# Optimization experiments

Measured on AMD Instinct MI355X. Metric: run time of the kernel, lower is better.

Reference implementation:

```python
import jax, jax.numpy as jnp
import numpy as np

NUM_HEADS = 32
NUM_KV_HEADS = 8
HEAD_DIM = 128  # hidden_size 4096 / 32 heads
ROPE_BASE = 10000.0


def setup_inputs() -> dict:
    key = jax.random.key(0)
    ks = jax.random.split(key, 5)
    H = NUM_HEADS * HEAD_DIM
    KV = NUM_KV_HEADS * HEAD_DIM
    B, S = 1, 2048
    s = 0.02
    return {
        "hidden_states": jax.random.normal(ks[0], (B, S, H), dtype=jnp.float32),
        "Wq": jax.random.normal(ks[1], (H, H), dtype=jnp.float32) * s,
        "Wk": jax.random.normal(ks[2], (H, KV), dtype=jnp.float32) * s,
        "Wv": jax.random.normal(ks[3], (H, KV), dtype=jnp.float32) * s,
        "Wo": jax.random.normal(ks[4], (H, H), dtype=jnp.float32) * s,
    }


def _rope_tables(seq_len, head_dim, dtype):
    inv_freq = 1.0 / (ROPE_BASE ** (jnp.arange(0, head_dim, 2, dtype=jnp.float32) / head_dim))
    freqs = jnp.arange(seq_len, dtype=jnp.float32)[:, None] * inv_freq[None, :]  # [S, hd/2]
    emb = jnp.concatenate([freqs, freqs], axis=-1)  # [S, hd]
    return emb.astype(dtype)  # angles; cos/sin taken by caller


def _rotate_half(x):
    x1, x2 = jnp.split(x, 2, axis=-1)
    return jnp.concatenate([-x2, x1], axis=-1)


def reference(hidden_states, Wq, Wk, Wv, Wo):
    B, S, H = hidden_states.shape
    hd = HEAD_DIM
    scale = hd ** -0.5

    q = (hidden_states @ Wq).reshape(B, S, NUM_HEADS, hd).transpose(0, 2, 1, 3)      # [B,nh,S,hd]
    k = (hidden_states @ Wk).reshape(B, S, NUM_KV_HEADS, hd).transpose(0, 2, 1, 3)   # [B,nkv,S,hd]
    v = (hidden_states @ Wv).reshape(B, S, NUM_KV_HEADS, hd).transpose(0, 2, 1, 3)

    ang = _rope_tables(S, hd, hidden_states.dtype)          # [S, hd]
    cos = jnp.cos(ang)[None, None]                          # [1,1,S,hd]
    sin = jnp.sin(ang)[None, None]
    q = q * cos + _rotate_half(q) * sin
    k = k * cos + _rotate_half(k) * sin

    rep = NUM_HEADS // NUM_KV_HEADS
    if rep > 1:
        k = jnp.repeat(k, rep, axis=1)  # matches torch repeat_interleave on head dim
        v = jnp.repeat(v, rep, axis=1)

    scores = jnp.einsum("bhqd,bhkd->bhqk", q, k) * scale    # [B,nh,S,S]
    causal = jnp.triu(jnp.ones((S, S), dtype=bool), k=1)
    scores = jnp.where(causal[None, None], jnp.float32(-jnp.inf).astype(scores.dtype), scores)
    weights = jax.nn.softmax(scores, axis=-1)
    attn = jnp.einsum("bhqk,bhkd->bhqd", weights, v)        # [B,nh,S,hd]
    out = attn.transpose(0, 2, 1, 3).reshape(B, S, H) @ Wo  # [B,S,H]
    return (out, k, v)
```

## Files before the change

kernel.cpp:

```cpp
#include <hip/hip_runtime.h>
#include <hip/hip_bf16.h>
#include <math.h>

typedef __bf16 bf16_t;
typedef bf16_t bf16x8 __attribute__((ext_vector_type(8)));
typedef bf16_t bf16x4 __attribute__((ext_vector_type(4)));
typedef float  f32x4  __attribute__((ext_vector_type(4)));

#define AS1(p) ((__attribute__((address_space(1))) void*)(p))
#define AS3(p) ((__attribute__((address_space(3))) void*)(p))

__global__ void convert_f32_bf16(const float* __restrict__ in, bf16_t* __restrict__ out)
{
    int i = blockIdx.x * 256 + threadIdx.x;
    float4 v = ((const float4*)in)[i];
    bf16x4 o;
    o[0] = (bf16_t)v.x; o[1] = (bf16_t)v.y; o[2] = (bf16_t)v.z; o[3] = (bf16_t)v.w;
    ((bf16x4*)out)[i] = o;
}

__global__ void transpose_convert(const float* __restrict__ W, bf16_t* __restrict__ Wt,
                                  int K, int N)
{
    __shared__ float tile[32][33];
    const int n0 = blockIdx.x * 32;
    const int k0 = blockIdx.y * 32;
    const int r = threadIdx.x >> 5;
    const int c = threadIdx.x & 31;
    #pragma unroll
    for (int i = 0; i < 32; i += 8)
        tile[r + i][c] = W[(size_t)(k0 + r + i) * N + n0 + c];
    __syncthreads();
    #pragma unroll
    for (int i = 0; i < 32; i += 8)
        Wt[(size_t)(n0 + r + i) * K + k0 + c] = (bf16_t)tile[c][r + i];
}

template <typename OutT>
__global__ __launch_bounds__(512, 2)
void gemm_bt_256(const bf16_t* __restrict__ A, const bf16_t* __restrict__ Bt,
                 OutT* __restrict__ C, int M, int N, int K)
{
    __shared__ __align__(16) bf16_t As[2 * 256 * 64];
    __shared__ __align__(16) bf16_t Bs[2 * 256 * 64];

    const int tid  = threadIdx.x;
    const int wave = tid >> 6;
    const int lane = tid & 63;
    const int lm = lane & 15, lq = lane >> 4;
    const int wr = wave >> 2, wc = wave & 3;
    const int m0 = blockIdx.x * 256;
    const int n0 = blockIdx.y * 256;

    const int sr = tid >> 3;
    const int sg = ((tid & 7) ^ (sr & 7)) * 8;
    char* Ab = (char*)As;
    char* Bb = (char*)Bs;
    const int fl = lm * 128 + ((lq ^ (lm & 7)) << 4);

    const int NT = K >> 6;

#define STAGE_A(buf, kt, h) do {                                                              \
    const bf16_t* _g0 = A + (size_t)(m0 + (h) * 128 + sr) * K + (kt) * 64 + sg;               \
    const bf16_t* _g1 = A + (size_t)(m0 + (h) * 128 + 64 + sr) * K + (kt) * 64 + sg;          \
    __builtin_amdgcn_global_load_lds(AS1(_g0),                                                \
        AS3(Ab + (buf) * 32768 + ((h) * 128 + wave * 8) * 128), 16, 0, 0);                    \
    __builtin_amdgcn_global_load_lds(AS1(_g1),                                                \
        AS3(Ab + (buf) * 32768 + ((h) * 128 + 64 + wave * 8) * 128), 16, 0, 0);               \
} while (0)
#define STAGE_B(buf, kt, h) do {                                                              \
    const bf16_t* _g0 = Bt + (size_t)(n0 + (h) * 128 + sr) * K + (kt) * 64 + sg;              \
    const bf16_t* _g1 = Bt + (size_t)(n0 + (h) * 128 + 64 + sr) * K + (kt) * 64 + sg;         \
    __builtin_amdgcn_global_load_lds(AS1(_g0),                                                \
        AS3(Bb + (buf) * 32768 + ((h) * 128 + wave * 8) * 128), 16, 0, 0);                    \
    __builtin_amdgcn_global_load_lds(AS1(_g1),                                                \
        AS3(Bb + (buf) * 32768 + ((h) * 128 + 64 + wave * 8) * 128), 16, 0, 0);               \
} while (0)

    f32x4 acc[8][4] = {};

    STAGE_A(0, 0, 0); STAGE_A(0, 0, 1);
    STAGE_B(0, 0, 0); STAGE_B(0, 0, 1);
    if (NT > 1) STAGE_A(1, 1, 0);
    asm volatile("s_waitcnt vmcnt(2)" ::: "memory");
    __builtin_amdgcn_s_barrier();

    int cur = 0;
    for (int kt = 0; kt < NT; ++kt) {
        const int nxt = cur ^ 1;
        const char* Ac = Ab + cur * 32768;
        const char* Bc = Bb + cur * 32768;
        bf16x8 a0[4][2], a1[4][2], b0[2][2], b1[2][2];

        #pragma unroll
        for (int mf = 0; mf < 4; ++mf)
            #pragma unroll
            for (int kk = 0; kk < 2; ++kk)
                a0[mf][kk] = *(const bf16x8*)(Ac + (wr * 128 + mf * 16) * 128 + (fl ^ (kk << 6)));
        #pragma unroll
        for (int nf = 0; nf < 2; ++nf)
            #pragma unroll
            for (int kk = 0; kk < 2; ++kk)
                b0[nf][kk] = *(const bf16x8*)(Bc + (wc * 64 + nf * 16) * 128 + (fl ^ (kk << 6)));
        if (kt + 1 < NT) { STAGE_A(nxt, kt + 1, 1); STAGE_B(nxt, kt + 1, 0); }
        __builtin_amdgcn_s_barrier();
        asm volatile("s_waitcnt lgkmcnt(0)" ::: "memory");
        __builtin_amdgcn_s_setprio(1);
        #pragma unroll
        for (int mf = 0; mf < 4; ++mf)
            #pragma unroll
            for (int nf = 0; nf < 2; ++nf)
                #pragma unroll
                for (int kk = 0; kk < 2; ++kk)
                    acc[mf][nf] = __builtin_amdgcn_mfma_f32_16x16x32_bf16(
                        a0[mf][kk], b0[nf][kk], acc[mf][nf], 0, 0, 0);
        __builtin_amdgcn_s_setprio(0);
        __builtin_amdgcn_s_barrier();

        #pragma unroll
        for (int nf = 0; nf < 2; ++nf)
            #pragma unroll
            for (int kk = 0; kk < 2; ++kk)
                b1[nf][kk] = *(const bf16x8*)(Bc + (wc * 64 + 32 + nf * 16) * 128 + (fl ^ (kk << 6)));
        if (kt + 1 < NT) STAGE_B(nxt, kt + 1, 1);
        __builtin_amdgcn_s_barrier();
        asm volatile("s_waitcnt lgkmcnt(0)" ::: "memory");
        __builtin_amdgcn_s_setprio(1);
        #pragma unroll
        for (int mf = 0; mf < 4; ++mf)
            #pragma unroll
            for (int nf = 0; nf < 2; ++nf)
                #pragma unroll
                for (int kk = 0; kk < 2; ++kk)
                    acc[mf][2 + nf] = __builtin_amdgcn_mfma_f32_16x16x32_bf16(
                        a0[mf][kk], b1[nf][kk], acc[mf][2 + nf], 0, 0, 0);
        __builtin_amdgcn_s_setprio(0);
        __builtin_amdgcn_s_barrier();

        #pragma unroll
        for (int mf = 0; mf < 4; ++mf)
            #pragma unroll
            for (int kk = 0; kk < 2; ++kk)
                a1[mf][kk] = *(const bf16x8*)(Ac + (wr * 128 + 64 + mf * 16) * 128 + (fl ^ (kk << 6)));
        __builtin_amdgcn_s_barrier();
        asm volatile("s_waitcnt lgkmcnt(0)" ::: "memory");
        __builtin_amdgcn_s_setprio(1);
        #pragma unroll
        for (int mf = 0; mf < 4; ++mf)
            #pragma unroll
            for (int nf = 0; nf < 2; ++nf)
                #pragma unroll
                for (int kk = 0; kk < 2; ++kk)
                    acc[4 + mf][nf] = __builtin_amdgcn_mfma_f32_16x16x32_bf16(
                        a1[mf][kk], b0[nf][kk], acc[4 + mf][nf], 0, 0, 0);
        __builtin_amdgcn_s_setprio(0);
        __builtin_amdgcn_s_barrier();

        if (kt + 2 < NT) {
            STAGE_A(cur, kt + 2, 0);
            asm volatile("s_waitcnt vmcnt(2)" ::: "memory");
        } else {
            asm volatile("s_waitcnt vmcnt(0)" ::: "memory");
        }
        __builtin_amdgcn_s_barrier();
        __builtin_amdgcn_s_setprio(1);
        #pragma unroll
        for (int mf = 0; mf < 4; ++mf)
            #pragma unroll
            for (int nf = 0; nf < 2; ++nf)
                #pragma unroll
                for (int kk = 0; kk < 2; ++kk)
                    acc[4 + mf][2 + nf] = __builtin_amdgcn_mfma_f32_16x16x32_bf16(
                        a1[mf][kk], b1[nf][kk], acc[4 + mf][2 + nf], 0, 0, 0);
        __builtin_amdgcn_s_setprio(0);
        __builtin_amdgcn_s_barrier();
        cur = nxt;
    }
#undef STAGE_A
#undef STAGE_B

    #pragma unroll
    for (int mi = 0; mi < 8; ++mi) {
        #pragma unroll
        for (int ni = 0; ni < 4; ++ni) {
            const int row = m0 + wr * 128 + mi * 16 + lq * 4;
            const int col = n0 + wc * 64 + ni * 16 + lm;
            #pragma unroll
            for (int r = 0; r < 4; ++r) {
                float v = acc[mi][ni][r];
                if constexpr (sizeof(OutT) == 2)
                    C[(size_t)(row + r) * N + col] = (OutT)(bf16_t)v;
                else
                    C[(size_t)(row + r) * N + col] = v;
            }
        }
    }
}

__global__ void rope_qk(bf16_t* __restrict__ QKV, float* __restrict__ k_out, int S)
{
    int idx  = blockIdx.x * 256 + threadIdx.x;
    int d    = idx & 63;
    int s    = idx >> 6;
    int head = blockIdx.y;
    float ang = (float)s * exp2f((float)d * -0.20762050593f);
    float sn, cs;
    sincosf(ang, &sn, &cs);
    int col = head < 32 ? head * 128 : 4096 + (head - 32) * 128;
    bf16_t* p = QKV + (size_t)s * 6144 + col;
    float x1 = (float)p[d], x2 = (float)p[d + 64];
    float y1 = x1 * cs - x2 * sn;
    float y2 = x2 * cs + x1 * sn;
    p[d]      = (bf16_t)y1;
    p[d + 64] = (bf16_t)y2;
    if (head >= 32) {
        int g = head - 32;
        #pragma unroll
        for (int j = 0; j < 4; ++j) {
            float* kb = k_out + ((size_t)(g * 4 + j) * S + s) * 128;
            kb[d]      = y1;
            kb[d + 64] = y2;
        }
    }
}

__global__ void v_finish(const bf16_t* __restrict__ QKV, float* __restrict__ v_out,
                         bf16_t* __restrict__ Vt, int S)
{
    __shared__ bf16_t tl[32][33];
    const int s0  = blockIdx.x * 32;
    const int gd0 = blockIdx.y * 32;
    const int r = threadIdx.x >> 5;
    const int c = threadIdx.x & 31;
    #pragma unroll
    for (int i = 0; i < 32; i += 8) {
        int s = s0 + r + i;
        bf16_t v = QKV[(size_t)s * 6144 + 5120 + gd0 + c];
        tl[r + i][c] = v;
        int gd = gd0 + c;
        int g = gd >> 7, d = gd & 127;
        float vf = (float)v;
        #pragma unroll
        for (int j = 0; j < 4; ++j)
            v_out[((size_t)(g * 4 + j) * S + s) * 128 + d] = vf;
    }
    __syncthreads();
    #pragma unroll
    for (int i = 0; i < 32; i += 8)
        Vt[(size_t)(gd0 + r + i) * S + s0 + c] = tl[c][r + i];
}

__global__ void pack_frags(const bf16_t* __restrict__ QKV, const bf16_t* __restrict__ Vt,
                           bf16_t* __restrict__ Kfrag, bf16_t* __restrict__ Vfrag, int S)
{
    const int b  = blockIdx.x;
    const int g  = b >> 5, kt = b & 31;
    const int t  = threadIdx.x;
    bf16x8* Kf = (bf16x8*)Kfrag + (size_t)b * 1024;
    bf16x8* Vf = (bf16x8*)Vfrag + (size_t)b * 1024;
    #pragma unroll
    for (int i = 0; i < 4; ++i) {
        int slot = i * 256 + t;
        int f = slot >> 6, l = slot & 63;
        int kk = f >> 2, nt = f & 3, lm = l & 15, lq = l >> 4;
        Kf[slot] = *(const bf16x8*)(QKV + (size_t)(kt * 64 + nt * 16 + lm) * 6144
                                    + 4096 + g * 128 + kk * 32 + lq * 8);
    }
    #pragma unroll
    for (int i = 0; i < 4; ++i) {
        int slot = i * 256 + t;
        int f = slot >> 6, l = slot & 63;
        int kk = f >> 3, nt = f & 7, lm = l & 15, lq = l >> 4;
        Vf[slot] = *(const bf16x8*)(Vt + (size_t)(g * 128 + nt * 16 + lm) * S
                                    + kt * 64 + kk * 32 + lq * 8);
    }
}

__global__ __launch_bounds__(64, 2)
void attn_fwd(const bf16_t* __restrict__ QKV,
              const bf16_t* __restrict__ Kfrag, const bf16_t* __restrict__ Vfrag,
              bf16_t* __restrict__ O, int S)
{
    const int task = blockIdx.x;
    const int h    = task & 31;
    const int c    = 63 - (task >> 5);
    const int g    = h >> 2;
    const int lane = threadIdx.x;
    const int lm   = lane & 15;
    const int lq   = lane >> 4;
    const int q0   = c * 32;

    __shared__ bf16_t P[32 * 72];

    bf16x8 aq[2][4];
    #pragma unroll
    for (int mi = 0; mi < 2; ++mi) {
        const bf16_t* qrow = QKV + (size_t)(q0 + mi * 16 + lm) * 6144 + h * 128;
        #pragma unroll
        for (int kk = 0; kk < 4; ++kk)
            aq[mi][kk] = *(const bf16x8*)(qrow + kk * 32 + lq * 8);
    }

    f32x4 acc[2][8] = {};
    float mrow[2][4], lrow[2][4];
    #pragma unroll
    for (int mi = 0; mi < 2; ++mi)
        #pragma unroll
        for (int r = 0; r < 4; ++r) { mrow[mi][r] = -3.0e38f; lrow[mi][r] = 0.f; }
    const float scale = 0.08838834764831845f;

    const int nkt = (q0 >> 6) + 1;

    for (int kt = 0; kt < nkt; ++kt) {
        const int k0 = kt * 64;
        const bf16x8* Kf = (const bf16x8*)Kfrag + ((size_t)(g * 32 + kt) << 10);
        const bf16x8* Vf = (const bf16x8*)Vfrag + ((size_t)(g * 32 + kt) << 10);

        bf16x8 bk[4][4];
        #pragma unroll
        for (int kk = 0; kk < 4; ++kk)
            #pragma unroll
            for (int nt = 0; nt < 4; ++nt)
                bk[kk][nt] = Kf[(kk * 4 + nt) * 64 + lane];

        f32x4 sc[2][4] = {};
        #pragma unroll
        for (int kk = 0; kk < 4; ++kk)
            #pragma unroll
            for (int nt = 0; nt < 4; ++nt)
                #pragma unroll
                for (int mi = 0; mi < 2; ++mi)
                    sc[mi][nt] = __builtin_amdgcn_mfma_f32_16x16x32_bf16(
                        aq[mi][kk], bk[kk][nt], sc[mi][nt], 0, 0, 0);

        bf16x8 bv[2][8];
        #pragma unroll
        for (int kk = 0; kk < 2; ++kk)
            #pragma unroll
            for (int nt = 0; nt < 8; ++nt)
                bv[kk][nt] = Vf[(kk * 8 + nt) * 64 + lane];

        #pragma unroll
        for (int mi = 0; mi < 2; ++mi)
            #pragma unroll
            for (int nt = 0; nt < 4; ++nt)
                #pragma unroll
                for (int r = 0; r < 4; ++r)
                    sc[mi][nt][r] *= scale;

        if (kt == nkt - 1) {
            #pragma unroll
            for (int mi = 0; mi < 2; ++mi)
                #pragma unroll
                for (int nt = 0; nt < 4; ++nt) {
                    int col = k0 + nt * 16 + lm;
                    #pragma unroll
                    for (int r = 0; r < 4; ++r) {
                        int row = q0 + mi * 16 + lq * 4 + r;
                        if (col > row) sc[mi][nt][r] = -3.0e38f;
                    }
                }
        }

        #pragma unroll
        for (int mi = 0; mi < 2; ++mi) {
            float tmax[4];
            #pragma unroll
            for (int r = 0; r < 4; ++r)
                tmax[r] = fmaxf(fmaxf(sc[mi][0][r], sc[mi][1][r]),
                                fmaxf(sc[mi][2][r], sc[mi][3][r]));
            #pragma unroll
            for (int off = 1; off < 16; off <<= 1)
                #pragma unroll
                for (int r = 0; r < 4; ++r)
                    tmax[r] = fmaxf(tmax[r], __shfl_xor(tmax[r], off));

            float alpha[4];
            #pragma unroll
            for (int r = 0; r < 4; ++r) {
                float mn = fmaxf(mrow[mi][r], tmax[r]);
                alpha[r] = __expf(mrow[mi][r] - mn);
                mrow[mi][r] = mn;
            }
            float rsum[4] = {0.f, 0.f, 0.f, 0.f};
            #pragma unroll
            for (int nt = 0; nt < 4; ++nt)
                #pragma unroll
                for (int r = 0; r < 4; ++r) {
                    float p = __expf(sc[mi][nt][r] - mrow[mi][r]);
                    sc[mi][nt][r] = p;
                    rsum[r] += p;
                }
            #pragma unroll
            for (int off = 1; off < 16; off <<= 1)
                #pragma unroll
                for (int r = 0; r < 4; ++r)
                    rsum[r] += __shfl_xor(rsum[r], off);
            #pragma unroll
            for (int r = 0; r < 4; ++r)
                lrow[mi][r] = lrow[mi][r] * alpha[r] + rsum[r];
            #pragma unroll
            for (int nt = 0; nt < 8; ++nt)
                #pragma unroll
                for (int r = 0; r < 4; ++r)
                    acc[mi][nt][r] *= alpha[r];

            #pragma unroll
            for (int nt = 0; nt < 4; ++nt)
                #pragma unroll
                for (int r = 0; r < 4; ++r)
                    P[(mi * 16 + lq * 4 + r) * 72 + nt * 16 + lm] = (bf16_t)sc[mi][nt][r];
        }

        bf16x8 ap[2][2];
        #pragma unroll
        for (int mi = 0; mi < 2; ++mi)
            #pragma unroll
            for (int kk = 0; kk < 2; ++kk)
                ap[mi][kk] = *(const bf16x8*)(P + (mi * 16 + lm) * 72 + kk * 32 + lq * 8);

        #pragma unroll
        for (int kk = 0; kk < 2; ++kk)
            #pragma unroll
            for (int nt = 0; nt < 8; ++nt)
                #pragma unroll
                for (int mi = 0; mi < 2; ++mi)
                    acc[mi][nt] = __builtin_amdgcn_mfma_f32_16x16x32_bf16(
                        ap[mi][kk], bv[kk][nt], acc[mi][nt], 0, 0, 0);
    }

    #pragma unroll
    for (int mi = 0; mi < 2; ++mi) {
        float inv[4];
        #pragma unroll
        for (int r = 0; r < 4; ++r) inv[r] = 1.0f / lrow[mi][r];
        #pragma unroll
        for (int nt = 0; nt < 8; ++nt)
            #pragma unroll
            for (int r = 0; r < 4; ++r) {
                int row = q0 + mi * 16 + lq * 4 + r;
                O[(size_t)row * 4096 + h * 128 + nt * 16 + lm] =
                    (bf16_t)(acc[mi][nt][r] * inv[r]);
            }
    }
}

extern "C" void kernel_launch(void* const* d_in, const int* in_sizes, int n_in,
                              void* d_out, int out_size, void* d_ws, size_t ws_size,
                              hipStream_t stream)
{
    const float* hidden = (const float*)d_in[0];
    const float* Wq = (const float*)d_in[1];
    const float* Wk = (const float*)d_in[2];
    const float* Wv = (const float*)d_in[3];
    const float* Wo = (const float*)d_in[4];

    const int S = 2048, H = 4096, KV = 1024, NQKV = 6144;

    char* ws = (char*)d_ws;
    bf16_t* hid_b  = (bf16_t*)(ws);
    bf16_t* Wqkv_t = (bf16_t*)(ws + (size_t)(16u  << 20));
    bf16_t* Wo_t   = (bf16_t*)(ws + (size_t)(64u  << 20));
    bf16_t* QKV    = (bf16_t*)(ws + (size_t)(96u  << 20));
    bf16_t* Vt     = (bf16_t*)(ws + (size_t)(120u << 20));
    bf16_t* attn   = (bf16_t*)(ws + (size_t)(124u << 20));
    bf16_t* Kfrag  = (bf16_t*)(ws);
    bf16_t* Vfrag  = (bf16_t*)(ws + (size_t)(4u << 20));

    float* out_o = (float*)d_out;
    float* out_k = out_o + (size_t)S * H;
    float* out_v = out_k + (size_t)32 * S * 128;

    convert_f32_bf16<<<S * H / 4 / 256, 256, 0, stream>>>(hidden, hid_b);
    transpose_convert<<<dim3(H / 32, H / 32), 256, 0, stream>>>(Wq, Wqkv_t, H, H);
    transpose_convert<<<dim3(KV / 32, H / 32), 256, 0, stream>>>(Wk, Wqkv_t + (size_t)4096 * H, H, KV);
    transpose_convert<<<dim3(KV / 32, H / 32), 256, 0, stream>>>(Wv, Wqkv_t + (size_t)5120 * H, H, KV);
    transpose_convert<<<dim3(H / 32, H / 32), 256, 0, stream>>>(Wo, Wo_t, H, H);

    gemm_bt_256<bf16_t><<<dim3(S / 256, NQKV / 256), 512, 0, stream>>>(hid_b, Wqkv_t, QKV, S, NQKV, H);

    rope_qk<<<dim3(S * 64 / 256, 40), 256, 0, stream>>>(QKV, out_k, S);
    v_finish<<<dim3(S / 32, KV / 32), 256, 0, stream>>>(QKV, out_v, Vt, S);
    pack_frags<<<256, 256, 0, stream>>>(QKV, Vt, Kfrag, Vfrag, S);

    attn_fwd<<<2048, 64, 0, stream>>>(QKV, Kfrag, Vfrag, attn, S);

    gemm_bt_256<float><<<dim3(S / 256, H / 256), 512, 0, stream>>>(attn, Wo_t, out_o, S, H, H);
}
```

Measured before the change: 660.7 us.

## Split-K the output projection GEMM and restage the GEMM prefetch pipeline

```diff
diff --git a/kernel.cpp b/kernel.cpp
--- a/kernel.cpp
+++ b/kernel.cpp
@@ -19,6 +19,16 @@
     ((bf16x4*)out)[i] = o;
 }
 
+__global__ void add_f32(const float* __restrict__ a, const float* __restrict__ b,
+                        float* __restrict__ o)
+{
+    int i = blockIdx.x * 256 + threadIdx.x;
+    float4 x = ((const float4*)a)[i];
+    float4 y = ((const float4*)b)[i];
+    x.x += y.x; x.y += y.y; x.z += y.z; x.w += y.w;
+    ((float4*)o)[i] = x;
+}
+
 __global__ void transpose_convert(const float* __restrict__ W, bf16_t* __restrict__ Wt,
                                   int K, int N)
 {
@@ -39,7 +49,7 @@
 template <typename OutT>
 __global__ __launch_bounds__(512, 2)
 void gemm_bt_256(const bf16_t* __restrict__ A, const bf16_t* __restrict__ Bt,
-                 OutT* __restrict__ C, int M, int N, int K)
+                 OutT* __restrict__ C, int M, int N, int Kc, int Kld)
 {
     __shared__ __align__(16) bf16_t As[2 * 256 * 64];
     __shared__ __align__(16) bf16_t Bs[2 * 256 * 64];
@@ -51,6 +61,9 @@
     const int wr = wave >> 2, wc = wave & 3;
     const int m0 = blockIdx.x * 256;
     const int n0 = blockIdx.y * 256;
+    A  += (size_t)blockIdx.z * Kc;
+    Bt += (size_t)blockIdx.z * Kc;
+    C  += (size_t)blockIdx.z * M * N;
 
     const int sr = tid >> 3;
     const int sg = ((tid & 7) ^ (sr & 7)) * 8;
@@ -58,36 +71,40 @@
     char* Bb = (char*)Bs;
     const int fl = lm * 128 + ((lq ^ (lm & 7)) << 4);
 
-    const int NT = K >> 6;
+    const int NT = Kc >> 6;
 
 #define STAGE_A(buf, kt, h) do {                                                              \
-    const bf16_t* _g0 = A + (size_t)(m0 + (h) * 128 + sr) * K + (kt) * 64 + sg;               \
-    const bf16_t* _g1 = A + (size_t)(m0 + (h) * 128 + 64 + sr) * K + (kt) * 64 + sg;          \
+    const bf16_t* _g0 = A + (size_t)(m0 + (h) * 128 + sr) * Kld + (kt) * 64 + sg;             \
+    const bf16_t* _g1 = A + (size_t)(m0 + (h) * 128 + 64 + sr) * Kld + (kt) * 64 + sg;        \
     __builtin_amdgcn_global_load_lds(AS1(_g0),                                                \
         AS3(Ab + (buf) * 32768 + ((h) * 128 + wave * 8) * 128), 16, 0, 0);                    \
     __builtin_amdgcn_global_load_lds(AS1(_g1),                                                \
         AS3(Ab + (buf) * 32768 + ((h) * 128 + 64 + wave * 8) * 128), 16, 0, 0);               \
 } while (0)
 #define STAGE_B(buf, kt, h) do {                                                              \
-    const bf16_t* _g0 = Bt + (size_t)(n0 + (h) * 128 + sr) * K + (kt) * 64 + sg;              \
-    const bf16_t* _g1 = Bt + (size_t)(n0 + (h) * 128 + 64 + sr) * K + (kt) * 64 + sg;         \
+    const bf16_t* _g0 = Bt + (size_t)(n0 + (h) * 128 + sr) * Kld + (kt) * 64 + sg;            \
+    const bf16_t* _g1 = Bt + (size_t)(n0 + (h) * 128 + 64 + sr) * Kld + (kt) * 64 + sg;       \
     __builtin_amdgcn_global_load_lds(AS1(_g0),                                                \
         AS3(Bb + (buf) * 32768 + ((h) * 128 + wave * 8) * 128), 16, 0, 0);                    \
     __builtin_amdgcn_global_load_lds(AS1(_g1),                                                \
         AS3(Bb + (buf) * 32768 + ((h) * 128 + 64 + wave * 8) * 128), 16, 0, 0);               \
 } while (0)
+#define STAGE_TILE(buf, kt) do {                                                              \
+    STAGE_A(buf, kt, 0); STAGE_A(buf, kt, 1);                                                 \
+    STAGE_B(buf, kt, 0); STAGE_B(buf, kt, 1);                                                 \
+} while (0)
 
     f32x4 acc[8][4] = {};
 
-    STAGE_A(0, 0, 0); STAGE_A(0, 0, 1);
-    STAGE_B(0, 0, 0); STAGE_B(0, 0, 1);
-    if (NT > 1) STAGE_A(1, 1, 0);
-    asm volatile("s_waitcnt vmcnt(2)" ::: "memory");
-    __builtin_amdgcn_s_barrier();
+    STAGE_TILE(0, 0);
+    if (NT > 1) STAGE_TILE(1, 1);
 
     int cur = 0;
     for (int kt = 0; kt < NT; ++kt) {
-        const int nxt = cur ^ 1;
+        if (kt + 1 < NT) asm volatile("s_waitcnt vmcnt(8)" ::: "memory");
+        else             asm volatile("s_waitcnt vmcnt(0)" ::: "memory");
+        __builtin_amdgcn_s_barrier();
+
         const char* Ac = Ab + cur * 32768;
         const char* Bc = Bb + cur * 32768;
         bf16x8 a0[4][2], a1[4][2], b0[2][2], b1[2][2];
@@ -102,7 +119,6 @@
             #pragma unroll
             for (int kk = 0; kk < 2; ++kk)
                 b0[nf][kk] = *(const bf16x8*)(Bc + (wc * 64 + nf * 16) * 128 + (fl ^ (kk << 6)));
-        if (kt + 1 < NT) { STAGE_A(nxt, kt + 1, 1); STAGE_B(nxt, kt + 1, 0); }
         __builtin_amdgcn_s_barrier();
         asm volatile("s_waitcnt lgkmcnt(0)" ::: "memory");
         __builtin_amdgcn_s_setprio(1);
@@ -122,7 +138,6 @@
             #pragma unroll
             for (int kk = 0; kk < 2; ++kk)
                 b1[nf][kk] = *(const bf16x8*)(Bc + (wc * 64 + 32 + nf * 16) * 128 + (fl ^ (kk << 6)));
-        if (kt + 1 < NT) STAGE_B(nxt, kt + 1, 1);
         __builtin_amdgcn_s_barrier();
         asm volatile("s_waitcnt lgkmcnt(0)" ::: "memory");
         __builtin_amdgcn_s_setprio(1);
@@ -156,13 +171,7 @@
         __builtin_amdgcn_s_setprio(0);
         __builtin_amdgcn_s_barrier();
 
-        if (kt + 2 < NT) {
-            STAGE_A(cur, kt + 2, 0);
-            asm volatile("s_waitcnt vmcnt(2)" ::: "memory");
-        } else {
-            asm volatile("s_waitcnt vmcnt(0)" ::: "memory");
-        }
-        __builtin_amdgcn_s_barrier();
+        if (kt + 2 < NT) STAGE_TILE(cur, kt + 2);
         __builtin_amdgcn_s_setprio(1);
         #pragma unroll
         for (int mf = 0; mf < 4; ++mf)
@@ -173,11 +182,11 @@
                     acc[4 + mf][2 + nf] = __builtin_amdgcn_mfma_f32_16x16x32_bf16(
                         a1[mf][kk], b1[nf][kk], acc[4 + mf][2 + nf], 0, 0, 0);
         __builtin_amdgcn_s_setprio(0);
-        __builtin_amdgcn_s_barrier();
-        cur = nxt;
+        cur ^= 1;
     }
 #undef STAGE_A
 #undef STAGE_B
+#undef STAGE_TILE
 
     #pragma unroll
     for (int mi = 0; mi < 8; ++mi) {
@@ -466,6 +475,7 @@
     bf16_t* attn   = (bf16_t*)(ws + (size_t)(124u << 20));
     bf16_t* Kfrag  = (bf16_t*)(ws);
     bf16_t* Vfrag  = (bf16_t*)(ws + (size_t)(4u << 20));
+    float* slab0   = (float*)(ws);
 
     float* out_o = (float*)d_out;
     float* out_k = out_o + (size_t)S * H;
@@ -477,7 +487,8 @@
     transpose_convert<<<dim3(KV / 32, H / 32), 256, 0, stream>>>(Wv, Wqkv_t + (size_t)5120 * H, H, KV);
     transpose_convert<<<dim3(H / 32, H / 32), 256, 0, stream>>>(Wo, Wo_t, H, H);
 
-    gemm_bt_256<bf16_t><<<dim3(S / 256, NQKV / 256), 512, 0, stream>>>(hid_b, Wqkv_t, QKV, S, NQKV, H);
+    gemm_bt_256<bf16_t><<<dim3(S / 256, NQKV / 256, 1), 512, 0, stream>>>(
+        hid_b, Wqkv_t, QKV, S, NQKV, H, H);
 
     rope_qk<<<dim3(S * 64 / 256, 40), 256, 0, stream>>>(QKV, out_k, S);
     v_finish<<<dim3(S / 32, KV / 32), 256, 0, stream>>>(QKV, out_v, Vt, S);
@@ -485,5 +496,7 @@
 
     attn_fwd<<<2048, 64, 0, stream>>>(QKV, Kfrag, Vfrag, attn, S);
 
-    gemm_bt_256<float><<<dim3(S / 256, H / 256), 512, 0, stream>>>(attn, Wo_t, out_o, S, H, H);
-}
+    gemm_bt_256<float><<<dim3(S / 256, H / 256, 2), 512, 0, stream>>>(
+        attn, Wo_t, slab0, S, H, H / 2, H);
+    add_f32<<<S * H / 4 / 256, 256, 0, stream>>>(slab0, slab0 + (size_t)S * H, out_o);
+}
```

Result: faster. 647.5 us (-2.0%).
